# Performance work log

Measured on AMD Instinct MI355X. Metric: run time of the kernel, lower is better.

## Reference

```python
import jax, jax.numpy as jnp
import numpy as np

ALPHA = 0.2        # LeakyReLU negative slope
MASK_VAL = -9e15   # matches torch -9000000000000000.0


def setup_inputs() -> dict:
    key = jax.random.key(0)
    k_h, k_adj, k_w, k_a = jax.random.split(key, 4)
    B, N, Nodes, IF, OF = 8, 8, 512, 256, 256
    h = jax.random.normal(k_h, (B, N, Nodes, IF), dtype=jnp.float32)
    adj = jax.random.randint(k_adj, (Nodes, Nodes), 0, 2, dtype=jnp.int32)
    # xavier_uniform with gain=1.414
    gain = 1.414
    lim_w = gain * np.sqrt(6.0 / (IF + OF))
    W = jax.random.uniform(k_w, (IF, OF), dtype=jnp.float32, minval=-lim_w, maxval=lim_w)
    lim_a = gain * np.sqrt(6.0 / (2 * OF + 1))
    a = jax.random.uniform(k_a, (2 * OF, 1), dtype=jnp.float32, minval=-lim_a, maxval=lim_a)
    return {"h": h, "adj": adj, "W": W, "a": a}


def reference(h, adj, W, a):
    # Wh: [B, N, Nodes, OF]
    Wh = jnp.matmul(h, W)
    OF = W.shape[1]
    a1, a2 = a[:OF, 0], a[OF:, 0]
    # e[..., i, j] = leakyrelu(a1 . Wh_i + a2 . Wh_j)  (decomposed additive attention)
    src = jnp.einsum('bnif,f->bni', Wh, a1)  # [B, N, Nodes]
    dst = jnp.einsum('bnjf,f->bnj', Wh, a2)  # [B, N, Nodes]
    e = jax.nn.leaky_relu(src[..., :, None] + dst[..., None, :], negative_slope=ALPHA)
    attention = jnp.where(adj > 0, e, jnp.full_like(e, MASK_VAL))
    attention = jax.nn.softmax(attention, axis=-1)
    # dropout is identity in eval mode (training=False)
    h_prime = jnp.matmul(attention, Wh)  # [B, N, Nodes, OF]
    return jax.nn.elu(h_prime)  # concat=True
```

## Files before the change

kernel.cpp:

```cpp
#include <hip/hip_runtime.h>
#include <hip/hip_bf16.h>


#define ALPHA 0.2f
#define MASK_VAL -9000000000000000.0f
#define NODES 512
#define FDIM 256
#define BN 64
#define SWZ(f) ((((f) ^ ((f) >> 2))) & 3)

typedef float  f32x4 __attribute__((ext_vector_type(4)));
typedef int    i32x4 __attribute__((ext_vector_type(4)));
typedef short  s16x8 __attribute__((ext_vector_type(8)));
typedef short  s16x4 __attribute__((ext_vector_type(4)));
typedef __bf16 bf16x8 __attribute__((ext_vector_type(8)));

__device__ __forceinline__ unsigned short f2bfu(float x) {
    __hip_bfloat16 b = __float2bfloat16(x);
    unsigned short u; __builtin_memcpy(&u, &b, 2); return u;
}
__device__ __forceinline__ float bfu2f(unsigned short u) {
    unsigned int w = ((unsigned int)u) << 16; return __uint_as_float(w);
}
__device__ __forceinline__ f32x4 mfma16(s16x8 a, s16x8 b, f32x4 c) {
    return __builtin_amdgcn_mfma_f32_16x16x32_bf16(
        __builtin_bit_cast(bf16x8, a), __builtin_bit_cast(bf16x8, b), c, 0, 0, 0);
}

__device__ __forceinline__ void split8v(f32x4 v0, f32x4 v1, s16x8& hi, s16x8& lo)
{
    float x[8] = {v0[0], v0[1], v0[2], v0[3], v1[0], v1[1], v1[2], v1[3]};
    unsigned hw[4], lw[4];
    #pragma unroll
    for (int d = 0; d < 4; ++d) {
        const unsigned u0 = __float_as_uint(x[2*d]);
        const unsigned u1 = __float_as_uint(x[2*d + 1]);
        hw[d] = __builtin_amdgcn_perm(u1, u0, 0x07060302);
        const float l0 = x[2*d]     - __uint_as_float(u0 & 0xFFFF0000u);
        const float l1 = x[2*d + 1] - __uint_as_float(u1 & 0xFFFF0000u);
        lw[d] = __builtin_amdgcn_perm(__float_as_uint(l1), __float_as_uint(l0),
                                      0x07060302);
    }
    hi = __builtin_bit_cast(s16x8, *(unsigned(*)[4])hw);
    lo = __builtin_bit_cast(s16x8, *(unsigned(*)[4])lw);
}

__device__ __forceinline__ void gll16(const void* g, void* l) {
    __builtin_amdgcn_global_load_lds(
        (const __attribute__((address_space(1))) unsigned int*)g,
        (__attribute__((address_space(3))) unsigned int*)l,
        16, 0, 0);
}

__global__ __launch_bounds__(256) void detect_kernel(const unsigned short* __restrict__ hraw,
                                                     int* __restrict__ flag)
{
    const int tid = threadIdx.x;
    float m = 0.0f;
    for (int i = tid; i < 16384; i += 256) {
        unsigned int w = ((unsigned int)hraw[i]) << 16;
        float v = __uint_as_float(w);
        v = fabsf(v);
        if (!(v == v)) v = 1e30f;
        m = fmaxf(m, v);
    }
    #pragma unroll
    for (int off = 32; off >= 1; off >>= 1)
        m = fmaxf(m, __shfl_down(m, off));
    __shared__ float red[4];
    if ((tid & 63) == 0) red[tid >> 6] = m;
    __syncthreads();
    if (tid == 0) {
        float mm = fmaxf(fmaxf(red[0], red[1]), fmaxf(red[2], red[3]));
        *flag = (mm > 1e4f) ? 1 : 0;
    }
}

__global__ __launch_bounds__(256) void prep_w_kernel(
    const void* __restrict__ Wv, const int* __restrict__ flagp,
    short* __restrict__ WtHi, short* __restrict__ WtLo)
{
    const int flag = *flagp;
    __shared__ float tile[16][17];
    const int tx = threadIdx.x & 15, ty = threadIdx.x >> 4;
    const int kk = blockIdx.y * 16 + ty;
    const int f  = blockIdx.x * 16 + tx;
    float v;
    if (flag) v = ((const float*)Wv)[kk * FDIM + f];
    else      v = bfu2f(((const unsigned short*)Wv)[kk * FDIM + f]);
    tile[ty][tx] = v;
    __syncthreads();
    const float x = tile[tx][ty];
    const int fo = blockIdx.x * 16 + ty;
    const int ko = blockIdx.y * 16 + tx;
    unsigned short h = f2bfu(x);
    WtHi[fo * FDIM + ko] = (short)h;
    WtLo[fo * FDIM + ko] = (short)f2bfu(x - bfu2f(h));
}

__global__ __launch_bounds__(256, 2) void wh_gemm(
    const void* __restrict__ hv,
    const short* __restrict__ WtHi, const short* __restrict__ WtLo,
    const void* __restrict__ av, const int* __restrict__ flagp,
    short* __restrict__ WhTHi, short* __restrict__ WhTLo,
    float* __restrict__ srcv, float* __restrict__ dstv)
{
    __shared__ __align__(16) char smem[81920];

    const int flag = *flagp;
    const int blk = blockIdx.x;
    const int bn  = blk >> 3;
    const int i0  = (blk & 7) * 64;
    const size_t r0g = (size_t)blk * 64;
    const int tid = threadIdx.x;
    const int w = tid >> 6, l = tid & 63;
    const int fb = l & 15, g = l >> 4;

    const int arow = tid >> 2, asg = tid & 3;
    const int aseg = asg ^ ((arow >> 1) & 3);
    const int awr  = arow * 64 + asg * 16;

    const short* gBh[4];
    const short* gBl[4];
    int bdst[4];
    {
        const int bsg = tid & 3;
        #pragma unroll
        for (int i = 0; i < 4; ++i) {
            const int f = i * 64 + (tid >> 2);
            const int ss = bsg ^ SWZ(f);
            gBh[i] = WtHi + f * FDIM + ss * 8;
            gBl[i] = WtLo + f * FDIM + ss * 8;
            bdst[i] = (i * 256 + tid) * 16;
        }
    }

    f32x4 acc[4][4];
    #pragma unroll
    for (int rt = 0; rt < 4; ++rt)
        #pragma unroll
        for (int ct = 0; ct < 4; ++ct) acc[rt][ct] = f32x4{0.f,0.f,0.f,0.f};

    if (flag) {
        const float* gA = (const float*)hv + (r0g + arow) * FDIM + aseg * 8;
        {
            f32x4 v0 = *(const f32x4*)gA;
            f32x4 v1 = *(const f32x4*)(gA + 4);
            #pragma unroll
            for (int i = 0; i < 4; ++i) {
                gll16(gBh[i], smem + 16384 + bdst[i]);
                gll16(gBl[i], smem + 49152 + bdst[i]);
            }
            s16x8 hi, lo; split8v(v0, v1, hi, lo);
            *(s16x8*)(smem + awr) = hi;
            *(s16x8*)(smem + 4096 + awr) = lo;
        }
        __syncthreads();
        for (int t = 0; t < 8; ++t) {
            const int cur = t & 1, nxt = cur ^ 1;
            f32x4 v0 = {}, v1 = {};
            if (t < 7) {
                v0 = *(const f32x4*)(gA + (t+1)*32);
                v1 = *(const f32x4*)(gA + (t+1)*32 + 4);
                #pragma unroll
                for (int i = 0; i < 4; ++i) {
                    gll16(gBh[i] + (t+1)*32, smem + 16384 + nxt*16384 + bdst[i]);
                    gll16(gBl[i] + (t+1)*32, smem + 49152 + nxt*16384 + bdst[i]);
                }
            }
            s16x8 bh[4], bl[4], ah[4], al[4];
            #pragma unroll
            for (int ct = 0; ct < 4; ++ct) {
                const int f = w*64 + ct*16 + fb;
                const int slot = g ^ SWZ(f);
                const int off = 16384 + cur*16384 + f*64 + slot*16;
                bh[ct] = *(const s16x8*)(smem + off);
                bl[ct] = *(const s16x8*)(smem + off + 32768);
            }
            #pragma unroll
            for (int rt = 0; rt < 4; ++rt) {
                const int row = rt*16 + fb;
                const int slot = g ^ ((row >> 1) & 3);
                const int off = cur*8192 + row*64 + slot*16;
                ah[rt] = *(const s16x8*)(smem + off);
                al[rt] = *(const s16x8*)(smem + off + 4096);
            }
            __builtin_amdgcn_s_setprio(1);
            #pragma unroll
            for (int rt = 0; rt < 4; ++rt)
                #pragma unroll
                for (int ct = 0; ct < 4; ++ct) {
                    acc[rt][ct] = mfma16(ah[rt], bh[ct], acc[rt][ct]);
                    acc[rt][ct] = mfma16(al[rt], bh[ct], acc[rt][ct]);
                    acc[rt][ct] = mfma16(ah[rt], bl[ct], acc[rt][ct]);
                }
            __builtin_amdgcn_s_setprio(0);
            if (t < 7) {
                s16x8 hi, lo; split8v(v0, v1, hi, lo);
                *(s16x8*)(smem + nxt*8192 + awr) = hi;
                *(s16x8*)(smem + nxt*8192 + 4096 + awr) = lo;
            }
            __syncthreads();
        }
    } else {
        const short* gA = (const short*)hv + (r0g + arow) * FDIM + aseg * 8;
        {
            s16x8 a0 = *(const s16x8*)gA;
            #pragma unroll
            for (int i = 0; i < 4; ++i) gll16(gBh[i], smem + 16384 + bdst[i]);
            *(s16x8*)(smem + awr) = a0;
        }
        __syncthreads();
        for (int t = 0; t < 8; ++t) {
            const int cur = t & 1, nxt = cur ^ 1;
            s16x8 an = {};
            if (t < 7) {
                an = *(const s16x8*)(gA + (t+1)*32);
                #pragma unroll
                for (int i = 0; i < 4; ++i)
                    gll16(gBh[i] + (t+1)*32, smem + 16384 + nxt*16384 + bdst[i]);
            }
            s16x8 bh[4], ah[4];
            #pragma unroll
            for (int ct = 0; ct < 4; ++ct) {
                const int f = w*64 + ct*16 + fb;
                const int slot = g ^ SWZ(f);
                bh[ct] = *(const s16x8*)(smem + 16384 + cur*16384 + f*64 + slot*16);
            }
            #pragma unroll
            for (int rt = 0; rt < 4; ++rt) {
                const int row = rt*16 + fb;
                const int slot = g ^ ((row >> 1) & 3);
                ah[rt] = *(const s16x8*)(smem + cur*8192 + row*64 + slot*16);
            }
            __builtin_amdgcn_s_setprio(1);
            #pragma unroll
            for (int rt = 0; rt < 4; ++rt)
                #pragma unroll
                for (int ct = 0; ct < 4; ++ct)
                    acc[rt][ct] = mfma16(ah[rt], bh[ct], acc[rt][ct]);
            __builtin_amdgcn_s_setprio(0);
            if (t < 7) *(s16x8*)(smem + nxt*8192 + awr) = an;
            __syncthreads();
        }
    }

    const size_t wbT = (size_t)bn * FDIM * NODES;
    #pragma unroll
    for (int rt = 0; rt < 4; ++rt) {
        const int orow = i0 + rt * 16 + g * 4;
        #pragma unroll
        for (int ct = 0; ct < 4; ++ct) {
            const int f = w * 64 + ct * 16 + fb;
            s16x4 h4, l4;
            #pragma unroll
            for (int r = 0; r < 4; ++r) {
                float x = acc[rt][ct][r];
                unsigned short hh = f2bfu(x);
                h4[r] = (short)hh;
                l4[r] = (short)f2bfu(x - bfu2f(hh));
            }
            *(s16x4*)(WhTHi + wbT + (size_t)f * NODES + orow) = h4;
            *(s16x4*)(WhTLo + wbT + (size_t)f * NODES + orow) = l4;
        }
    }

    float a1v[4], a2v[4];
    #pragma unroll
    for (int ct = 0; ct < 4; ++ct) {
        const int f = w * 64 + ct * 16 + fb;
        if (flag) {
            a1v[ct] = ((const float*)av)[f];
            a2v[ct] = ((const float*)av)[FDIM + f];
        } else {
            a1v[ct] = bfu2f(((const unsigned short*)av)[f]);
            a2v[ct] = bfu2f(((const unsigned short*)av)[FDIM + f]);
        }
    }
    float* red1 = (float*)smem;
    float* red2 = red1 + 256;
    #pragma unroll
    for (int rt = 0; rt < 4; ++rt) {
        #pragma unroll
        for (int r = 0; r < 4; ++r) {
            float s1 = 0.f, s2 = 0.f;
            #pragma unroll
            for (int ct = 0; ct < 4; ++ct) {
                s1 = fmaf(acc[rt][ct][r], a1v[ct], s1);
                s2 = fmaf(acc[rt][ct][r], a2v[ct], s2);
            }
            #pragma unroll
            for (int off = 1; off <= 8; off <<= 1) {
                s1 += __shfl_xor(s1, off);
                s2 += __shfl_xor(s2, off);
            }
            if (fb == 0) {
                red1[w * 64 + rt * 16 + g * 4 + r] = s1;
                red2[w * 64 + rt * 16 + g * 4 + r] = s2;
            }
        }
    }
    __syncthreads();
    if (tid < 64) {
        srcv[bn * NODES + i0 + tid] =
            red1[tid] + red1[64 + tid] + red1[128 + tid] + red1[192 + tid];
        dstv[bn * NODES + i0 + tid] =
            red2[tid] + red2[64 + tid] + red2[128 + tid] + red2[192 + tid];
    }
}

__global__ __launch_bounds__(512, 2) void pv_gemm(
    const short* __restrict__ WhTHi, const short* __restrict__ WhTLo,
    const float* __restrict__ srcv, const float* __restrict__ dstv,
    const int* __restrict__ adj, const int* __restrict__ flagp,
    void* __restrict__ out)
{
    __shared__ __align__(16) char smem[163840];

    const int flag = *flagp;
    const int b0 = blockIdx.x;
    const int blk = (b0 & 7) * 64 + (b0 >> 3);
    const int bn  = blk >> 3;
    const int i0  = (blk & 7) * 64;
    const int tid = threadIdx.x;
    const int w = tid >> 6, l = tid & 63;

    const short* bhig = WhTHi + (size_t)bn * FDIM * NODES;
    const short* blog = WhTLo + (size_t)bn * FDIM * NODES;

    const int sf0 = w * 32 + (l >> 2);
    const int sf1 = sf0 + 16;
    const int sl  = l & 3;
    const short* gH0 = bhig + (size_t)sf0 * NODES + (sl ^ SWZ(sf0)) * 8;
    const short* gH1 = bhig + (size_t)sf1 * NODES + (sl ^ SWZ(sf1)) * 8;
    const short* gL0 = blog + (size_t)sf0 * NODES + (sl ^ SWZ(sf0)) * 8;
    const short* gL1 = blog + (size_t)sf1 * NODES + (sl ^ SWZ(sf1)) * 8;
    const int dB = (w * 32) * 64 + l * 16;

    auto stage = [&](int buf, int t) {
        const int ko = t * 32;
        char* base = smem + 65536 + buf * 32768;
        gll16(gH0 + ko, base + dB);
        gll16(gH1 + ko, base + dB + 1024);
        gll16(gL0 + ko, base + 16384 + dB);
        gll16(gL1 + ko, base + 16384 + dB + 1024);
    };

    stage(0, 0);
    stage(1, 1);

    {
        const float* drow = dstv + bn * NODES;
        const int j = l * 8;
        for (int rr = 0; rr < 8; ++rr) {
            const int r = w * 8 + rr;
            const int* adjrow = adj + (size_t)(i0 + r) * NODES;
            const float srow = srcv[bn * NODES + i0 + r];
            const i32x4 q0 = *(const i32x4*)(adjrow + j);
            const i32x4 q1 = *(const i32x4*)(adjrow + j + 4);
            const f32x4 d0 = *(const f32x4*)(drow + j);
            const f32x4 d1 = *(const f32x4*)(drow + j + 4);
            float e[8];
            #pragma unroll
            for (int k = 0; k < 4; ++k) {
                float ev = srow + d0[k];
                ev = (ev > 0.f) ? ev : ALPHA * ev;
                e[k] = (q0[k] > 0) ? ev : MASK_VAL;
                float ew = srow + d1[k];
                ew = (ew > 0.f) ? ew : ALPHA * ew;
                e[4 + k] = (q1[k] > 0) ? ew : MASK_VAL;
            }
            float m = e[0];
            #pragma unroll
            for (int k = 1; k < 8; ++k) m = fmaxf(m, e[k]);
            #pragma unroll
            for (int off = 1; off <= 32; off <<= 1) m = fmaxf(m, __shfl_xor(m, off));
            float p[8], s = 0.f;
            #pragma unroll
            for (int k = 0; k < 8; ++k) {
                p[k] = __expf(e[k] - m);
                s += p[k];
            }
            #pragma unroll
            for (int off = 1; off <= 32; off <<= 1) s += __shfl_xor(s, off);
            const float isum = 1.0f / s;
            s16x8 ph;
            #pragma unroll
            for (int k = 0; k < 8; ++k) ph[k] = (short)f2bfu(p[k] * isum);
            *(s16x8*)(smem + r * 1024 + ((l ^ (r & 7)) * 16)) = ph;
        }
    }
    asm volatile("s_waitcnt lgkmcnt(0)" ::: "memory");
    __builtin_amdgcn_s_barrier();

    const int fb = l & 15, g = l >> 4;

    unsigned boff[2];
    #pragma unroll
    for (int ct = 0; ct < 2; ++ct) {
        const int f = w * 32 + ct * 16 + fb;
        boff[ct] = (unsigned)(65536 + f * 64 + (g ^ SWZ(f)) * 16);
    }

    f32x4 acc[4][2];
    #pragma unroll
    for (int rt = 0; rt < 4; ++rt)
        #pragma unroll
        for (int ct = 0; ct < 2; ++ct) acc[rt][ct] = f32x4{0.f,0.f,0.f,0.f};

    int cur = 0;
    for (int t = 0; t < 16; ++t) {
        if (t < 14) {
            int nb = cur + 2; if (nb >= 3) nb -= 3;
            stage(nb, t + 2);
        }
        if (t < 14)       asm volatile("s_waitcnt vmcnt(8)" ::: "memory");
        else if (t == 14) asm volatile("s_waitcnt vmcnt(4)" ::: "memory");
        else              asm volatile("s_waitcnt vmcnt(0)" ::: "memory");

        const unsigned bbase = (unsigned)(cur * 32768);
        s16x8 bh[2], bl[2];
        #pragma unroll
        for (int ct = 0; ct < 2; ++ct) {
            bh[ct] = *(const s16x8*)(smem + bbase + boff[ct]);
            bl[ct] = *(const s16x8*)(smem + bbase + boff[ct] + 16384);
        }
        s16x8 af[4];
        #pragma unroll
        for (int rt = 0; rt < 4; ++rt) {
            const int row = rt * 16 + fb;
            const unsigned seg = (unsigned)(t * 4 + g) ^ (unsigned)(row & 7);
            af[rt] = *(const s16x8*)(smem + (unsigned)(row * 1024) + seg * 16);
        }
        __builtin_amdgcn_s_setprio(1);
        #pragma unroll
        for (int rt = 0; rt < 4; ++rt) {
            acc[rt][0] = mfma16(af[rt], bh[0], acc[rt][0]);
            acc[rt][0] = mfma16(af[rt], bl[0], acc[rt][0]);
            acc[rt][1] = mfma16(af[rt], bh[1], acc[rt][1]);
            acc[rt][1] = mfma16(af[rt], bl[1], acc[rt][1]);
        }
        __builtin_amdgcn_s_setprio(0);
        cur = cur + 1; if (cur == 3) cur = 0;
    }

    #pragma unroll
    for (int rt = 0; rt < 4; ++rt) {
        #pragma unroll
        for (int ct = 0; ct < 2; ++ct) {
            const int f = w * 32 + ct * 16 + fb;
            #pragma unroll
            for (int r = 0; r < 4; ++r) {
                float v = acc[rt][ct][r];
                v = (v > 0.f) ? v : expm1f(v);
                const size_t o = ((size_t)bn * NODES + i0 + rt * 16 + g * 4 + r) * FDIM + f;
                if (flag) ((float*)out)[o] = v;
                else      ((unsigned short*)out)[o] = f2bfu(v);
            }
        }
    }
}

extern "C" void kernel_launch(void* const* d_in, const int* in_sizes, int n_in,
                              void* d_out, int out_size, void* d_ws, size_t ws_size,
                              hipStream_t stream)
{
    const void* h   = d_in[0];
    const int*  adj = (const int*)d_in[1];
    const void* W   = d_in[2];
    const void* a   = d_in[3];

    int*   flag  = (int*)d_ws;
    float* srcv  = (float*)d_ws + 64;
    float* dstv  = srcv + BN * NODES;
    short* WtHi  = (short*)(dstv + BN * NODES);
    short* WtLo  = WtHi + FDIM * FDIM;
    short* WhTHi = WtLo + FDIM * FDIM;
    short* WhTLo = WhTHi + (size_t)BN * FDIM * NODES;

    detect_kernel<<<1, 256, 0, stream>>>((const unsigned short*)h, flag);
    prep_w_kernel<<<dim3(16, 16), 256, 0, stream>>>(W, flag, WtHi, WtLo);
    wh_gemm<<<512, 256, 0, stream>>>(h, WtHi, WtLo, a, flag,
                                     WhTHi, WhTLo, srcv, dstv);
    pv_gemm<<<512, 512, 0, stream>>>(WhTHi, WhTLo, srcv, dstv, adj, flag, d_out);
}
```

Measured before the change: 167.2 us.

## Read B operands straight from global memory and shrink LDS to raise occupancy

In wh_gemm the whole 64x256 A tile is staged into LDS once, with a new swizzle and no double buffering. The W operand fragments are now loaded directly from global memory into registers instead of going through LDS. pv_gemm likewise drops its triple-buffered LDS staging of WhT and loads B fragments from global inside the loop. LDS use is cut enough that launch bounds can raise pv_gemm to 4 blocks per CU. This removes LDS traffic, barriers and waitcnt management, but relies on cache hits and occupancy to hide global load latency. It also adds a stored per-row inverse sum.

```diff
diff --git a/kernel.cpp b/kernel.cpp
--- a/kernel.cpp
+++ b/kernel.cpp
@@ -7,7 +7,6 @@
 #define NODES 512
 #define FDIM 256
 #define BN 64
-#define SWZ(f) ((((f) ^ ((f) >> 2))) & 3)
 
 typedef float  f32x4 __attribute__((ext_vector_type(4)));
 typedef int    i32x4 __attribute__((ext_vector_type(4)));
@@ -105,7 +104,7 @@
     short* __restrict__ WhTHi, short* __restrict__ WhTLo,
     float* __restrict__ srcv, float* __restrict__ dstv)
 {
-    __shared__ __align__(16) char smem[81920];
+    __shared__ __align__(16) char smem[67584];
 
     const int flag = *flagp;
     const int blk = blockIdx.x;
@@ -116,24 +115,32 @@
     const int w = tid >> 6, l = tid & 63;
     const int fb = l & 15, g = l >> 4;
 
-    const int arow = tid >> 2, asg = tid & 3;
-    const int aseg = asg ^ ((arow >> 1) & 3);
-    const int awr  = arow * 64 + asg * 16;
-
-    const short* gBh[4];
-    const short* gBl[4];
-    int bdst[4];
-    {
-        const int bsg = tid & 3;
-        #pragma unroll
-        for (int i = 0; i < 4; ++i) {
-            const int f = i * 64 + (tid >> 2);
-            const int ss = bsg ^ SWZ(f);
-            gBh[i] = WtHi + f * FDIM + ss * 8;
-            gBl[i] = WtLo + f * FDIM + ss * 8;
-            bdst[i] = (i * 256 + tid) * 16;
-        }
-    }
+    if (flag) {
+        const int srow = tid >> 2, q = tid & 3;
+        const float* gA = (const float*)hv + (r0g + srow) * FDIM;
+        #pragma unroll
+        for (int i = 0; i < 8; ++i) {
+            const int seg = q + 4 * i;
+            f32x4 v0 = *(const f32x4*)(gA + seg * 8);
+            f32x4 v1 = *(const f32x4*)(gA + seg * 8 + 4);
+            s16x8 hi, lo; split8v(v0, v1, hi, lo);
+            const int slot = seg ^ (srow & 7);
+            *(s16x8*)(smem + srow * 512 + slot * 16) = hi;
+            *(s16x8*)(smem + 32768 + srow * 512 + slot * 16) = lo;
+        }
+    } else {
+        const short* hs = (const short*)hv;
+        const unsigned wub = (unsigned)(tid & ~63);
+        #pragma unroll
+        for (int i = 0; i < 8; ++i) {
+            const int idx = i * 256 + tid;
+            const int row = idx >> 5, slot = idx & 31;
+            const int srcseg = slot ^ (row & 7);
+            gll16(hs + (r0g + row) * FDIM + srcseg * 8,
+                  smem + (i * 256 + (int)wub) * 16);
+        }
+    }
+    __syncthreads();
 
     f32x4 acc[4][4];
     #pragma unroll
@@ -142,50 +149,22 @@
         for (int ct = 0; ct < 4; ++ct) acc[rt][ct] = f32x4{0.f,0.f,0.f,0.f};
 
     if (flag) {
-        const float* gA = (const float*)hv + (r0g + arow) * FDIM + aseg * 8;
-        {
-            f32x4 v0 = *(const f32x4*)gA;
-            f32x4 v1 = *(const f32x4*)(gA + 4);
-            #pragma unroll
-            for (int i = 0; i < 4; ++i) {
-                gll16(gBh[i], smem + 16384 + bdst[i]);
-                gll16(gBl[i], smem + 49152 + bdst[i]);
-            }
-            s16x8 hi, lo; split8v(v0, v1, hi, lo);
-            *(s16x8*)(smem + awr) = hi;
-            *(s16x8*)(smem + 4096 + awr) = lo;
-        }
-        __syncthreads();
+        #pragma unroll
         for (int t = 0; t < 8; ++t) {
-            const int cur = t & 1, nxt = cur ^ 1;
-            f32x4 v0 = {}, v1 = {};
-            if (t < 7) {
-                v0 = *(const f32x4*)(gA + (t+1)*32);
-                v1 = *(const f32x4*)(gA + (t+1)*32 + 4);
-                #pragma unroll
-                for (int i = 0; i < 4; ++i) {
-                    gll16(gBh[i] + (t+1)*32, smem + 16384 + nxt*16384 + bdst[i]);
-                    gll16(gBl[i] + (t+1)*32, smem + 49152 + nxt*16384 + bdst[i]);
-                }
-            }
             s16x8 bh[4], bl[4], ah[4], al[4];
             #pragma unroll
             for (int ct = 0; ct < 4; ++ct) {
-                const int f = w*64 + ct*16 + fb;
-                const int slot = g ^ SWZ(f);
-                const int off = 16384 + cur*16384 + f*64 + slot*16;
-                bh[ct] = *(const s16x8*)(smem + off);
-                bl[ct] = *(const s16x8*)(smem + off + 32768);
+                const int f = w * 64 + ct * 16 + fb;
+                bh[ct] = *(const s16x8*)(WtHi + f * FDIM + t * 32 + g * 8);
+                bl[ct] = *(const s16x8*)(WtLo + f * FDIM + t * 32 + g * 8);
             }
             #pragma unroll
             for (int rt = 0; rt < 4; ++rt) {
-                const int row = rt*16 + fb;
-                const int slot = g ^ ((row >> 1) & 3);
-                const int off = cur*8192 + row*64 + slot*16;
-                ah[rt] = *(const s16x8*)(smem + off);
-                al[rt] = *(const s16x8*)(smem + off + 4096);
-            }
-            __builtin_amdgcn_s_setprio(1);
+                const int row = rt * 16 + fb;
+                const int slot = (t * 4 + g) ^ (row & 7);
+                ah[rt] = *(const s16x8*)(smem + row * 512 + slot * 16);
+                al[rt] = *(const s16x8*)(smem + 32768 + row * 512 + slot * 16);
+            }
             #pragma unroll
             for (int rt = 0; rt < 4; ++rt)
                 #pragma unroll
@@ -194,54 +173,27 @@
                     acc[rt][ct] = mfma16(al[rt], bh[ct], acc[rt][ct]);
                     acc[rt][ct] = mfma16(ah[rt], bl[ct], acc[rt][ct]);
                 }
-            __builtin_amdgcn_s_setprio(0);
-            if (t < 7) {
-                s16x8 hi, lo; split8v(v0, v1, hi, lo);
-                *(s16x8*)(smem + nxt*8192 + awr) = hi;
-                *(s16x8*)(smem + nxt*8192 + 4096 + awr) = lo;
-            }
-            __syncthreads();
         }
     } else {
-        const short* gA = (const short*)hv + (r0g + arow) * FDIM + aseg * 8;
-        {
-            s16x8 a0 = *(const s16x8*)gA;
-            #pragma unroll
-            for (int i = 0; i < 4; ++i) gll16(gBh[i], smem + 16384 + bdst[i]);
-            *(s16x8*)(smem + awr) = a0;
-        }
-        __syncthreads();
+        #pragma unroll
         for (int t = 0; t < 8; ++t) {
-            const int cur = t & 1, nxt = cur ^ 1;
-            s16x8 an = {};
-            if (t < 7) {
-                an = *(const s16x8*)(gA + (t+1)*32);
-                #pragma unroll
-                for (int i = 0; i < 4; ++i)
-                    gll16(gBh[i] + (t+1)*32, smem + 16384 + nxt*16384 + bdst[i]);
-            }
             s16x8 bh[4], ah[4];
             #pragma unroll
             for (int ct = 0; ct < 4; ++ct) {
-                const int f = w*64 + ct*16 + fb;
-                const int slot = g ^ SWZ(f);
-                bh[ct] = *(const s16x8*)(smem + 16384 + cur*16384 + f*64 + slot*16);
+                const int f = w * 64 + ct * 16 + fb;
+                bh[ct] = *(const s16x8*)(WtHi + f * FDIM + t * 32 + g * 8);
             }
             #pragma unroll
             for (int rt = 0; rt < 4; ++rt) {
-                const int row = rt*16 + fb;
-                const int slot = g ^ ((row >> 1) & 3);
-                ah[rt] = *(const s16x8*)(smem + cur*8192 + row*64 + slot*16);
-            }
-            __builtin_amdgcn_s_setprio(1);
+                const int row = rt * 16 + fb;
+                const int slot = (t * 4 + g) ^ (row & 7);
+                ah[rt] = *(const s16x8*)(smem + row * 512 + slot * 16);
+            }
             #pragma unroll
             for (int rt = 0; rt < 4; ++rt)
                 #pragma unroll
                 for (int ct = 0; ct < 4; ++ct)
                     acc[rt][ct] = mfma16(ah[rt], bh[ct], acc[rt][ct]);
-            __builtin_amdgcn_s_setprio(0);
-            if (t < 7) *(s16x8*)(smem + nxt*8192 + awr) = an;
-            __syncthreads();
         }
     }
 
@@ -277,7 +229,7 @@
             a2v[ct] = bfu2f(((const unsigned short*)av)[FDIM + f]);
         }
     }
-    float* red1 = (float*)smem;
+    float* red1 = (float*)(smem + 65536);
     float* red2 = red1 + 256;
     #pragma unroll
     for (int rt = 0; rt < 4; ++rt) {
@@ -309,13 +261,13 @@
     }
 }
 
-__global__ __launch_bounds__(512, 2) void pv_gemm(
+__global__ __launch_bounds__(512, 4) void pv_gemm(
     const short* __restrict__ WhTHi, const short* __restrict__ WhTLo,
     const float* __restrict__ srcv, const float* __restrict__ dstv,
     const int* __restrict__ adj, const int* __restrict__ flagp,
     void* __restrict__ out)
 {
-    __shared__ __align__(16) char smem[163840];
+    __shared__ __align__(16) char smem[65792];
 
     const int flag = *flagp;
     const int b0 = blockIdx.x;
@@ -327,27 +279,7 @@
 
     const short* bhig = WhTHi + (size_t)bn * FDIM * NODES;
     const short* blog = WhTLo + (size_t)bn * FDIM * NODES;
-
-    const int sf0 = w * 32 + (l >> 2);
-    const int sf1 = sf0 + 16;
-    const int sl  = l & 3;
-    const short* gH0 = bhig + (size_t)sf0 * NODES + (sl ^ SWZ(sf0)) * 8;
-    const short* gH1 = bhig + (size_t)sf1 * NODES + (sl ^ SWZ(sf1)) * 8;
-    const short* gL0 = blog + (size_t)sf0 * NODES + (sl ^ SWZ(sf0)) * 8;
-    const short* gL1 = blog + (size_t)sf1 * NODES + (sl ^ SWZ(sf1)) * 8;
-    const int dB = (w * 32) * 64 + l * 16;
-
-    auto stage = [&](int buf, int t) {
-        const int ko = t * 32;
-        char* base = smem + 65536 + buf * 32768;
-        gll16(gH0 + ko, base + dB);
-        gll16(gH1 + ko, base + dB + 1024);
-        gll16(gL0 + ko, base + 16384 + dB);
-        gll16(gL1 + ko, base + 16384 + dB + 1024);
-    };
-
-    stage(0, 0);
-    stage(1, 1);
+    float* rowinvS = (float*)(smem + 65536);
 
     {
         const float* drow = dstv + bn * NODES;
@@ -388,19 +320,18 @@
             #pragma unroll
             for (int k = 0; k < 8; ++k) ph[k] = (short)f2bfu(p[k] * isum);
             *(s16x8*)(smem + r * 1024 + ((l ^ (r & 7)) * 16)) = ph;
-        }
-    }
-    asm volatile("s_waitcnt lgkmcnt(0)" ::: "memory");
-    __builtin_amdgcn_s_barrier();
+            if (l == 0) rowinvS[r] = isum;
+        }
+    }
+    __syncthreads();
 
     const int fb = l & 15, g = l >> 4;
-
-    unsigned boff[2];
-    #pragma unroll
-    for (int ct = 0; ct < 2; ++ct) {
-        const int f = w * 32 + ct * 16 + fb;
-        boff[ct] = (unsigned)(65536 + f * 64 + (g ^ SWZ(f)) * 16);
-    }
+    const int f0 = w * 32 + fb;
+    const int f1 = f0 + 16;
+    const short* gH0 = bhig + (size_t)f0 * NODES + g * 8;
+    const short* gH1 = bhig + (size_t)f1 * NODES + g * 8;
+    const short* gL0 = blog + (size_t)f0 * NODES + g * 8;
+    const short* gL1 = blog + (size_t)f1 * NODES + g * 8;
 
     f32x4 acc[4][2];
     #pragma unroll
@@ -408,23 +339,12 @@
         #pragma unroll
         for (int ct = 0; ct < 2; ++ct) acc[rt][ct] = f32x4{0.f,0.f,0.f,0.f};
 
-    int cur = 0;
+    #pragma unroll 4
     for (int t = 0; t < 16; ++t) {
-        if (t < 14) {
-            int nb = cur + 2; if (nb >= 3) nb -= 3;
-            stage(nb, t + 2);
-        }
-        if (t < 14)       asm volatile("s_waitcnt vmcnt(8)" ::: "memory");
-        else if (t == 14) asm volatile("s_waitcnt vmcnt(4)" ::: "memory");
-        else              asm volatile("s_waitcnt vmcnt(0)" ::: "memory");
-
-        const unsigned bbase = (unsigned)(cur * 32768);
-        s16x8 bh[2], bl[2];
-        #pragma unroll
-        for (int ct = 0; ct < 2; ++ct) {
-            bh[ct] = *(const s16x8*)(smem + bbase + boff[ct]);
-            bl[ct] = *(const s16x8*)(smem + bbase + boff[ct] + 16384);
-        }
+        s16x8 bh0 = *(const s16x8*)(gH0 + t * 32);
+        s16x8 bh1 = *(const s16x8*)(gH1 + t * 32);
+        s16x8 bl0 = *(const s16x8*)(gL0 + t * 32);
+        s16x8 bl1 = *(const s16x8*)(gL1 + t * 32);
         s16x8 af[4];
         #pragma unroll
         for (int rt = 0; rt < 4; ++rt) {
@@ -432,16 +352,13 @@
             const unsigned seg = (unsigned)(t * 4 + g) ^ (unsigned)(row & 7);
             af[rt] = *(const s16x8*)(smem + (unsigned)(row * 1024) + seg * 16);
         }
-        __builtin_amdgcn_s_setprio(1);
         #pragma unroll
         for (int rt = 0; rt < 4; ++rt) {
-            acc[rt][0] = mfma16(af[rt], bh[0], acc[rt][0]);
-            acc[rt][0] = mfma16(af[rt], bl[0], acc[rt][0]);
-            acc[rt][1] = mfma16(af[rt], bh[1], acc[rt][1]);
-            acc[rt][1] = mfma16(af[rt], bl[1], acc[rt][1]);
-        }
-        __builtin_amdgcn_s_setprio(0);
-        cur = cur + 1; if (cur == 3) cur = 0;
+            acc[rt][0] = mfma16(af[rt], bh0, acc[rt][0]);
+            acc[rt][0] = mfma16(af[rt], bl0, acc[rt][0]);
+            acc[rt][1] = mfma16(af[rt], bh1, acc[rt][1]);
+            acc[rt][1] = mfma16(af[rt], bl1, acc[rt][1]);
+        }
     }
 
     #pragma unroll
```

Result: no change. 169.9 us (+1.6%).
